# Kernel tuning notes

Measured on AMD Instinct MI355X. Metric: run time of the kernel, lower is better.

The kernel has to match this reference:

```python
import jax, jax.numpy as jnp
import numpy as np

KS = 7       # neighborhood kernel size (fixed in __init__)
HEADS = 8    # num_heads (fixed in __init__)
LN_EPS = 1e-5


def _nbr_idx(L, k):
    # NATTEN-style clamped window: window start shifts inward at borders (no padding)
    starts = jnp.clip(jnp.arange(L) - k // 2, 0, L - k)
    idx = starts[:, None] + jnp.arange(k)            # [L, k] absolute neighbor coords
    rel = idx - jnp.arange(L)[:, None] + (k - 1)     # [L, k] rel-pos-bias index in [0, 2k-2]
    return idx, rel


def _na2d(x, qkv_w, qkv_b, proj_w, proj_b, rpb):
    # x: [B, H, W, C]  -> neighborhood attention with clamped 7x7 windows
    B, H, W, C = x.shape
    hd = C // HEADS
    qkv = x @ qkv_w.T + qkv_b                        # [B,H,W,3C]
    q, k, v = jnp.split(qkv, 3, axis=-1)
    q = q.reshape(B, H, W, HEADS, hd) * (hd ** -0.5)
    k = k.reshape(B, H, W, HEADS, hd)
    v = v.reshape(B, H, W, HEADS, hd)
    ri, rri = _nbr_idx(H, KS)                        # [H,KS]
    ci, rci = _nbr_idx(W, KS)                        # [W,KS]
    # gather neighborhoods: [B,H,W,KS,KS,heads,hd]
    kn = k[:, ri[:, None, :, None], ci[None, :, None, :]]
    vn = v[:, ri[:, None, :, None], ci[None, :, None, :]]
    scores = jnp.einsum('bijhd,bijpqhd->bhijpq', q, kn)   # [B,heads,H,W,KS,KS]
    bias = rpb[:, rri[:, None, :, None], rci[None, :, None, :]]  # [heads,H,W,KS,KS]
    scores = scores + bias[None]
    attn = jax.nn.softmax(scores.reshape(B, HEADS, H, W, KS * KS), axis=-1)
    vn = vn.reshape(B, H, W, KS * KS, HEADS, hd)
    out = jnp.einsum('bhijp,bijphd->bijhd', attn, vn)      # [B,H,W,heads,hd]
    out = out.reshape(B, H, W, C)
    return out @ proj_w.T + proj_b


def _layernorm(x, g, b):
    mu = jnp.mean(x, axis=-1, keepdims=True)
    var = jnp.mean((x - mu) ** 2, axis=-1, keepdims=True)
    return (x - mu) * jax.lax.rsqrt(var + LN_EPS) * g + b


def setup_inputs() -> dict:
    key = jax.random.key(0)
    ks = jax.random.split(key, 4)
    B, T, H, W, C = 2, 8, 48, 48, 64
    return {
        'q': jax.random.normal(ks[0], (B, T, H, W, C), dtype=jnp.float32),
        'qkv_w': jax.random.normal(ks[1], (3 * C, C), dtype=jnp.float32) * 0.02,
        'qkv_b': jnp.zeros((3 * C,), jnp.float32),
        'proj_w': jax.random.normal(ks[2], (C, C), dtype=jnp.float32) * 0.02,
        'proj_b': jnp.zeros((C,), jnp.float32),
        'rpb': jax.random.normal(ks[3], (HEADS, 2 * KS - 1, 2 * KS - 1), dtype=jnp.float32) * 0.02,
        'ln_g': jnp.ones((C,), jnp.float32),
        'ln_b': jnp.zeros((C,), jnp.float32),
    }


def reference(q, qkv_w, qkv_b, proj_w, proj_b, rpb, ln_g, ln_b):
    B, T, H, W, C = q.shape
    x = q.reshape(B * T, H, W, C)                    # '(b t) h w c'
    x = _na2d(x, qkv_w, qkv_b, proj_w, proj_b, rpb)  # wPT path
    x = x.reshape(B, T, H, W, C)
    return _layernorm(x, ln_g, ln_b)                 # norm_q; wGC=False
```

## Files before the change

### kernel.cpp

```cpp
#include <hip/hip_runtime.h>
#include <hip/hip_bf16.h>

#define BT   16
#define IH   48
#define IW   48
#define CH   64
#define NH   8
#define HD   8
#define KS   7
#define NPIX (BT*IH*IW)
#define QKVC 192
#define LN_EPS 1e-5f
#define QSCALE 0.35355339059327373f

#define TSH  4
#define TSW  8
#define TP   (TSH*TSW)
#define AOS  72

typedef __bf16 bf16_t;
typedef bf16_t bf16x8 __attribute__((ext_vector_type(8)));
typedef float  f32x4  __attribute__((ext_vector_type(4)));
typedef float  f32x2  __attribute__((ext_vector_type(2)));

__device__ __forceinline__ float bflo(unsigned u) { union { unsigned i; float f; } v; v.i = u << 16; return v.f; }
__device__ __forceinline__ float bfhi(unsigned u) { union { unsigned i; float f; } v; v.i = u & 0xffff0000u; return v.f; }
__device__ __forceinline__ f32x2 unp2(unsigned u) { f32x2 r; r.x = bflo(u); r.y = bfhi(u); return r; }

__device__ __forceinline__ float4 ldf4u(const float* p) {
    float4 r; __builtin_memcpy(&r, p, 16); return r;
}

__device__ __forceinline__ bf16x8 pack_bf16x8(float4 lo, float4 hi) {
    bf16x8 r;
    r[0] = (bf16_t)lo.x; r[1] = (bf16_t)lo.y; r[2] = (bf16_t)lo.z; r[3] = (bf16_t)lo.w;
    r[4] = (bf16_t)hi.x; r[5] = (bf16_t)hi.y; r[6] = (bf16_t)hi.z; r[7] = (bf16_t)hi.w;
    return r;
}

__global__ __launch_bounds__(192) void qkv_kernel(
        const float* __restrict__ x,
        const float* __restrict__ w,
        const float* __restrict__ b,
        __hip_bfloat16* __restrict__ qkv) {
    const int mg   = blockIdx.x;
    const int ngrp = threadIdx.x >> 6;
    const int l  = threadIdx.x & 63;
    const int m  = l & 15;
    const int kg = l >> 4;

    const int ch_base = ngrp * 64 + m * 4;
    const float4 bias4 = *(const float4*)(b + ch_base);
    const float scale = (ngrp == 0) ? QSCALE : 1.f;

    bf16x8 wb0[4], wb1[4];
    #pragma unroll
    for (int t = 0; t < 4; ++t) {
        const float* wr_ = w + (size_t)(ch_base + t) * CH + kg * 8;
        wb0[t] = pack_bf16x8(*(const float4*)(wr_),      *(const float4*)(wr_ + 4));
        wb1[t] = pack_bf16x8(*(const float4*)(wr_ + 32), *(const float4*)(wr_ + 36));
    }

    #pragma unroll
    for (int mm = 0; mm < 2; ++mm) {
        const int mtile = mg * 2 + mm;
        const float* xr = x + (size_t)(mtile * 16 + m) * CH + kg * 8;
        const bf16x8 a0 = pack_bf16x8(*(const float4*)(xr),      *(const float4*)(xr + 4));
        const bf16x8 a1 = pack_bf16x8(*(const float4*)(xr + 32), *(const float4*)(xr + 36));

        float val[4][4];
        #pragma unroll
        for (int t = 0; t < 4; ++t) {
            f32x4 acc = {0.f, 0.f, 0.f, 0.f};
            acc = __builtin_amdgcn_mfma_f32_16x16x32_bf16(a0, wb0[t], acc, 0, 0, 0);
            acc = __builtin_amdgcn_mfma_f32_16x16x32_bf16(a1, wb1[t], acc, 0, 0, 0);
            const float bias = (t == 0) ? bias4.x : (t == 1) ? bias4.y : (t == 2) ? bias4.z : bias4.w;
            #pragma unroll
            for (int r = 0; r < 4; ++r) val[t][r] = (acc[r] + bias) * scale;
        }
        #pragma unroll
        for (int r = 0; r < 4; ++r) {
            const int pix = mtile * 16 + kg * 4 + r;
            union { ushort4 u; __hip_bfloat16 hh[4]; } pk;
            #pragma unroll
            for (int t = 0; t < 4; ++t) pk.hh[t] = __float2bfloat16(val[t][r]);
            *reinterpret_cast<ushort4*>(qkv + (size_t)pix * QKVC + ch_base) = pk.u;
        }
    }
}

__global__ __launch_bounds__(128) void attn_proj_ln_kernel(
        const __hip_bfloat16* __restrict__ qkv,
        const float* __restrict__ rpb,
        const float* __restrict__ pw,
        const float* __restrict__ pb,
        const float* __restrict__ g,
        const float* __restrict__ beta,
        float* __restrict__ out) {
    __shared__ __align__(16) __hip_bfloat16 ao[TP * AOS];

    const int blk  = blockIdx.x;
    const int n    = blk & 15;
    const int tile = blk >> 4;
    const int i0   = (tile / 6) * TSH;
    const int j0   = (tile % 6) * TSW;
    const int tid  = threadIdx.x;
    const size_t img = (size_t)n * (IH * IW);

    {
        const int h  = tid & 7;
        const int pr = tid >> 3;
        const int pi = pr >> 3;
        const int pj = pr & 7;
        const int i  = i0 + pi * 2;
        const int j  = j0 + pj;
        const int pl0 = pi * 16 + pj;
        const int pl1 = pl0 + 8;

        f32x2 q0[4], q1[4];
        {
            const uint4 u = *reinterpret_cast<const uint4*>(
                qkv + (img + i * IW + j) * QKVC + h * HD);
            q0[0] = unp2(u.x); q0[1] = unp2(u.y); q0[2] = unp2(u.z); q0[3] = unp2(u.w);
            const uint4 v = *reinterpret_cast<const uint4*>(
                qkv + (img + (i + 1) * IW + j) * QKVC + h * HD);
            q1[0] = unp2(v.x); q1[1] = unp2(v.y); q1[2] = unp2(v.z); q1[3] = unp2(v.w);
        }

        int si0 = i - 3;     si0 = si0 < 0 ? 0 : (si0 > IH - KS ? IH - KS : si0);
        int si1 = i - 2;     si1 = si1 < 0 ? 0 : (si1 > IH - KS ? IH - KS : si1);
        int sj  = j - 3;     sj  = sj  < 0 ? 0 : (sj  > IW - KS ? IW - KS : sj);
        const int off    = si1 - si0;
        const int rbase0 = si0 - i + 6;
        const float* rpc = rpb + h * (2*KS-1) * (2*KS-1) + (sj - j + (KS - 1));

        float lr0 = 0.f, lr1 = 0.f;
        f32x2 a0[4], a1[4];
        #pragma unroll
        for (int d = 0; d < 4; ++d) { a0[d] = (f32x2){0.f,0.f}; a1[d] = (f32x2){0.f,0.f}; }

        for (int p = 0; p < 8; ++p) {
            if (p == 7 && off == 0) break;
            const bool d0 = (p < 7);
            const bool d1 = (p > 0) || (off == 0);
            const __hip_bfloat16* row =
                qkv + (img + (si0 + p) * IW + sj) * QKVC + CH + h * HD;

            uint4 kb[KS], vb[KS];
            #pragma unroll
            for (int qq = 0; qq < KS; ++qq) {
                kb[qq] = *reinterpret_cast<const uint4*>(row + qq * QKVC);
                vb[qq] = *reinterpret_cast<const uint4*>(row + qq * QKVC + CH);
            }
            float4 r0a = {0,0,0,0}, r0b = {0,0,0,0}, r1a = {0,0,0,0}, r1b = {0,0,0,0};
            if (d0) {
                const float* rr = rpc + (rbase0 + p) * (2*KS-1);
                r0a = ldf4u(rr); r0b = ldf4u(rr + 3);
            }
            if (d1) {
                const float* rr = rpc + (rbase0 - 1 + p) * (2*KS-1);
                r1a = ldf4u(rr); r1b = ldf4u(rr + 3);
            }

            float s0[KS], s1[KS];
            #pragma unroll
            for (int qq = 0; qq < KS; ++qq) {
                const f32x2 k0 = unp2(kb[qq].x), k1 = unp2(kb[qq].y);
                const f32x2 k2 = unp2(kb[qq].z), k3 = unp2(kb[qq].w);
                f32x2 t0 = q0[0]*k0 + q0[1]*k1 + q0[2]*k2 + q0[3]*k3;
                f32x2 t1 = q1[0]*k0 + q1[1]*k1 + q1[2]*k2 + q1[3]*k3;
                s0[qq] = t0.x + t0.y;
                s1[qq] = t1.x + t1.y;
            }
            float e0[KS], e1[KS];
            #pragma unroll
            for (int qq = 0; qq < KS; ++qq) { e0[qq] = 0.f; e1[qq] = 0.f; }
            if (d0) {
                e0[0] = __expf(s0[0] + r0a.x); e0[1] = __expf(s0[1] + r0a.y);
                e0[2] = __expf(s0[2] + r0a.z); e0[3] = __expf(s0[3] + r0a.w);
                e0[4] = __expf(s0[4] + r0b.y); e0[5] = __expf(s0[5] + r0b.z);
                e0[6] = __expf(s0[6] + r0b.w);
            }
            if (d1) {
                e1[0] = __expf(s1[0] + r1a.x); e1[1] = __expf(s1[1] + r1a.y);
                e1[2] = __expf(s1[2] + r1a.z); e1[3] = __expf(s1[3] + r1a.w);
                e1[4] = __expf(s1[4] + r1b.y); e1[5] = __expf(s1[5] + r1b.z);
                e1[6] = __expf(s1[6] + r1b.w);
            }
            #pragma unroll
            for (int qq = 0; qq < KS; ++qq) {
                const f32x2 v0 = unp2(vb[qq].x), v1 = unp2(vb[qq].y);
                const f32x2 v2 = unp2(vb[qq].z), v3 = unp2(vb[qq].w);
                lr0 += e0[qq];
                a0[0] += e0[qq] * v0; a0[1] += e0[qq] * v1;
                a0[2] += e0[qq] * v2; a0[3] += e0[qq] * v3;
                lr1 += e1[qq];
                a1[0] += e1[qq] * v0; a1[1] += e1[qq] * v1;
                a1[2] += e1[qq] * v2; a1[3] += e1[qq] * v3;
            }
        }
        const float inv0 = 1.f / lr0;
        const float inv1 = 1.f / lr1;
        union { uint4 u; __hip_bfloat16 hh[8]; } pk;
        #pragma unroll
        for (int d = 0; d < 4; ++d) {
            pk.hh[2*d]   = __float2bfloat16(a0[d].x * inv0);
            pk.hh[2*d+1] = __float2bfloat16(a0[d].y * inv0);
        }
        *reinterpret_cast<uint4*>(ao + pl0 * AOS + h * HD) = pk.u;
        #pragma unroll
        for (int d = 0; d < 4; ++d) {
            pk.hh[2*d]   = __float2bfloat16(a1[d].x * inv1);
            pk.hh[2*d+1] = __float2bfloat16(a1[d].y * inv1);
        }
        *reinterpret_cast<uint4*>(ao + pl1 * AOS + h * HD) = pk.u;
    }
    __syncthreads();

    {
        const int wv = tid >> 6;
        const int l  = tid & 63;
        const int m  = l & 15;
        const int kg = l >> 4;

        const __hip_bfloat16* ar = ao + (wv * 16 + m) * AOS + kg * 8;
        const bf16x8 a0 = *reinterpret_cast<const bf16x8*>(ar);
        const bf16x8 a1 = *reinterpret_cast<const bf16x8*>(ar + 32);

        const int ch_base = m * 4;
        const float4 bias4 = *(const float4*)(pb + ch_base);

        float val[4][4];
        #pragma unroll
        for (int t = 0; t < 4; ++t) {
            const float* wr_ = pw + (size_t)(ch_base + t) * CH + kg * 8;
            const bf16x8 b0 = pack_bf16x8(*(const float4*)(wr_),      *(const float4*)(wr_ + 4));
            const bf16x8 b1 = pack_bf16x8(*(const float4*)(wr_ + 32), *(const float4*)(wr_ + 36));
            f32x4 acc = {0.f, 0.f, 0.f, 0.f};
            acc = __builtin_amdgcn_mfma_f32_16x16x32_bf16(a0, b0, acc, 0, 0, 0);
            acc = __builtin_amdgcn_mfma_f32_16x16x32_bf16(a1, b1, acc, 0, 0, 0);
            const float bias = (t == 0) ? bias4.x : (t == 1) ? bias4.y : (t == 2) ? bias4.z : bias4.w;
            #pragma unroll
            for (int r = 0; r < 4; ++r) val[t][r] = acc[r] + bias;
        }

        float sm[4];
        #pragma unroll
        for (int r = 0; r < 4; ++r) sm[r] = val[0][r] + val[1][r] + val[2][r] + val[3][r];
        #pragma unroll
        for (int mask = 1; mask <= 8; mask <<= 1) {
            #pragma unroll
            for (int r = 0; r < 4; ++r) sm[r] += __shfl_xor(sm[r], mask, 64);
        }
        float mu[4];
        #pragma unroll
        for (int r = 0; r < 4; ++r) mu[r] = sm[r] * (1.f / 64.f);

        float qs[4];
        #pragma unroll
        for (int r = 0; r < 4; ++r) {
            float a = val[0][r] - mu[r], bq = val[1][r] - mu[r];
            float c = val[2][r] - mu[r], d = val[3][r] - mu[r];
            qs[r] = a * a + bq * bq + c * c + d * d;
        }
        #pragma unroll
        for (int mask = 1; mask <= 8; mask <<= 1) {
            #pragma unroll
            for (int r = 0; r < 4; ++r) qs[r] += __shfl_xor(qs[r], mask, 64);
        }
        float rs[4];
        #pragma unroll
        for (int r = 0; r < 4; ++r) rs[r] = rsqrtf(qs[r] * (1.f / 64.f) + LN_EPS);

        const float4 g4  = *(const float4*)(g + ch_base);
        const float4 be4 = *(const float4*)(beta + ch_base);
        #pragma unroll
        for (int r = 0; r < 4; ++r) {
            const int pl = wv * 16 + kg * 4 + r;
            const int gi = i0 + (pl >> 3), gj = j0 + (pl & 7);
            float4 o;
            o.x = (val[0][r] - mu[r]) * rs[r] * g4.x + be4.x;
            o.y = (val[1][r] - mu[r]) * rs[r] * g4.y + be4.y;
            o.z = (val[2][r] - mu[r]) * rs[r] * g4.z + be4.z;
            o.w = (val[3][r] - mu[r]) * rs[r] * g4.w + be4.w;
            *reinterpret_cast<float4*>(out + (img + gi * IW + gj) * CH + ch_base) = o;
        }
    }
}

extern "C" void kernel_launch(void* const* d_in, const int* in_sizes, int n_in,
                              void* d_out, int out_size, void* d_ws, size_t ws_size,
                              hipStream_t stream) {
    const float* x      = (const float*)d_in[0];
    const float* qkv_w  = (const float*)d_in[1];
    const float* qkv_b  = (const float*)d_in[2];
    const float* proj_w = (const float*)d_in[3];
    const float* proj_b = (const float*)d_in[4];
    const float* rpb    = (const float*)d_in[5];
    const float* ln_g   = (const float*)d_in[6];
    const float* ln_b   = (const float*)d_in[7];
    float* out = (float*)d_out;

    __hip_bfloat16* qkv = (__hip_bfloat16*)d_ws;

    qkv_kernel<<<1152, 192, 0, stream>>>(x, qkv_w, qkv_b, qkv);
    attn_proj_ln_kernel<<<1152, 128, 0, stream>>>(qkv, rpb, proj_w, proj_b,
                                                  ln_g, ln_b, out);
}
```

Baseline: 111.9 us.

## Fuse QKV projection into attention kernel with halo-recomputed K/V in LDS

Merges the QKV projection and the attention/proj/LayerNorm kernels into one launch that works on 8x8 output tiles. Each block computes Q for its tile and K/V for a 14x14 halo region directly into shared memory, so the bf16 QKV round trip through global memory goes away. In exchange, K/V for halo pixels is recomputed by neighbouring tiles (about 3x redundant projection work), and the larger LDS footprint per block may limit occupancy. Tile size, block size and grid size change to match the new layout.

```diff
diff --git a/kernel.cpp b/kernel.cpp
--- a/kernel.cpp
+++ b/kernel.cpp
@@ -1,21 +1,17 @@
 #include <hip/hip_runtime.h>
 #include <hip/hip_bf16.h>
 
-#define BT   16
 #define IH   48
 #define IW   48
 #define CH   64
-#define NH   8
-#define HD   8
 #define KS   7
-#define NPIX (BT*IH*IW)
-#define QKVC 192
 #define LN_EPS 1e-5f
 #define QSCALE 0.35355339059327373f
 
-#define TSH  4
-#define TSW  8
-#define TP   (TSH*TSW)
+#define TS   8
+#define HS   14
+#define HP   196
+#define KVS  128
 #define AOS  72
 
 typedef __bf16 bf16_t;
@@ -38,74 +34,112 @@
     return r;
 }
 
-__global__ __launch_bounds__(192) void qkv_kernel(
+__global__ __launch_bounds__(256, 2) void fused_na_kernel(
         const float* __restrict__ x,
         const float* __restrict__ w,
         const float* __restrict__ b,
-        __hip_bfloat16* __restrict__ qkv) {
-    const int mg   = blockIdx.x;
-    const int ngrp = threadIdx.x >> 6;
-    const int l  = threadIdx.x & 63;
-    const int m  = l & 15;
-    const int kg = l >> 4;
-
-    const int ch_base = ngrp * 64 + m * 4;
-    const float4 bias4 = *(const float4*)(b + ch_base);
-    const float scale = (ngrp == 0) ? QSCALE : 1.f;
-
-    bf16x8 wb0[4], wb1[4];
-    #pragma unroll
-    for (int t = 0; t < 4; ++t) {
-        const float* wr_ = w + (size_t)(ch_base + t) * CH + kg * 8;
-        wb0[t] = pack_bf16x8(*(const float4*)(wr_),      *(const float4*)(wr_ + 4));
-        wb1[t] = pack_bf16x8(*(const float4*)(wr_ + 32), *(const float4*)(wr_ + 36));
-    }
-
-    #pragma unroll
-    for (int mm = 0; mm < 2; ++mm) {
-        const int mtile = mg * 2 + mm;
-        const float* xr = x + (size_t)(mtile * 16 + m) * CH + kg * 8;
-        const bf16x8 a0 = pack_bf16x8(*(const float4*)(xr),      *(const float4*)(xr + 4));
-        const bf16x8 a1 = pack_bf16x8(*(const float4*)(xr + 32), *(const float4*)(xr + 36));
-
-        float val[4][4];
-        #pragma unroll
-        for (int t = 0; t < 4; ++t) {
-            f32x4 acc = {0.f, 0.f, 0.f, 0.f};
-            acc = __builtin_amdgcn_mfma_f32_16x16x32_bf16(a0, wb0[t], acc, 0, 0, 0);
-            acc = __builtin_amdgcn_mfma_f32_16x16x32_bf16(a1, wb1[t], acc, 0, 0, 0);
-            const float bias = (t == 0) ? bias4.x : (t == 1) ? bias4.y : (t == 2) ? bias4.z : bias4.w;
-            #pragma unroll
-            for (int r = 0; r < 4; ++r) val[t][r] = (acc[r] + bias) * scale;
-        }
-        #pragma unroll
-        for (int r = 0; r < 4; ++r) {
-            const int pix = mtile * 16 + kg * 4 + r;
-            union { ushort4 u; __hip_bfloat16 hh[4]; } pk;
-            #pragma unroll
-            for (int t = 0; t < 4; ++t) pk.hh[t] = __float2bfloat16(val[t][r]);
-            *reinterpret_cast<ushort4*>(qkv + (size_t)pix * QKVC + ch_base) = pk.u;
-        }
-    }
-}
-
-__global__ __launch_bounds__(128) void attn_proj_ln_kernel(
-        const __hip_bfloat16* __restrict__ qkv,
         const float* __restrict__ rpb,
         const float* __restrict__ pw,
         const float* __restrict__ pb,
         const float* __restrict__ g,
         const float* __restrict__ beta,
         float* __restrict__ out) {
-    __shared__ __align__(16) __hip_bfloat16 ao[TP * AOS];
+    __shared__ __align__(16) __hip_bfloat16 kv[HP * KVS];
+    __shared__ __align__(16) __hip_bfloat16 qao[64 * AOS];
 
     const int blk  = blockIdx.x;
     const int n    = blk & 15;
     const int tile = blk >> 4;
-    const int i0   = (tile / 6) * TSH;
-    const int j0   = (tile % 6) * TSW;
-    const int tid  = threadIdx.x;
+    const int i0   = (tile / 6) * TS;
+    const int j0   = (tile % 6) * TS;
+    int h0 = i0 - 3; h0 = h0 < 0 ? 0 : (h0 > IH - HS ? IH - HS : h0);
+    int w0 = j0 - 3; w0 = w0 < 0 ? 0 : (w0 > IW - HS ? IW - HS : w0);
+    const int tid = threadIdx.x;
     const size_t img = (size_t)n * (IH * IW);
+
+    {
+        const int wv = tid >> 6;
+        const int l  = tid & 63;
+        const int m  = l & 15;
+        const int kg = l >> 4;
+
+        {
+            const int ch_base = m * 4;
+            const float4 bias4 = *(const float4*)(b + ch_base);
+            bf16x8 wb0[4], wb1[4];
+            #pragma unroll
+            for (int t = 0; t < 4; ++t) {
+                const float* wr_ = w + (size_t)(ch_base + t) * CH + kg * 8;
+                wb0[t] = pack_bf16x8(*(const float4*)(wr_),      *(const float4*)(wr_ + 4));
+                wb1[t] = pack_bf16x8(*(const float4*)(wr_ + 32), *(const float4*)(wr_ + 36));
+            }
+            const int px = wv * 16 + m;
+            const int hr = i0 + (px >> 3);
+            const int wc = j0 + (px & 7);
+            const float* xr = x + (img + hr * IW + wc) * CH + kg * 8;
+            const bf16x8 a0 = pack_bf16x8(*(const float4*)(xr),      *(const float4*)(xr + 4));
+            const bf16x8 a1 = pack_bf16x8(*(const float4*)(xr + 32), *(const float4*)(xr + 36));
+            float val[4][4];
+            #pragma unroll
+            for (int t = 0; t < 4; ++t) {
+                f32x4 acc = {0.f, 0.f, 0.f, 0.f};
+                acc = __builtin_amdgcn_mfma_f32_16x16x32_bf16(a0, wb0[t], acc, 0, 0, 0);
+                acc = __builtin_amdgcn_mfma_f32_16x16x32_bf16(a1, wb1[t], acc, 0, 0, 0);
+                const float bias = (t == 0) ? bias4.x : (t == 1) ? bias4.y : (t == 2) ? bias4.z : bias4.w;
+                #pragma unroll
+                for (int rr = 0; rr < 4; ++rr) val[t][rr] = (acc[rr] + bias) * QSCALE;
+            }
+            #pragma unroll
+            for (int rr = 0; rr < 4; ++rr) {
+                const int pix = wv * 16 + kg * 4 + rr;
+                union { ushort4 u; __hip_bfloat16 hh[4]; } pk;
+                #pragma unroll
+                for (int t = 0; t < 4; ++t) pk.hh[t] = __float2bfloat16(val[t][rr]);
+                *reinterpret_cast<ushort4*>(qao + pix * 64 + ch_base) = pk.u;
+            }
+        }
+
+        for (int grp = 1; grp < 3; ++grp) {
+            const int ch_base = grp * 64 + m * 4;
+            const float4 bias4 = *(const float4*)(b + ch_base);
+            bf16x8 wb0[4], wb1[4];
+            #pragma unroll
+            for (int t = 0; t < 4; ++t) {
+                const float* wr_ = w + (size_t)(ch_base + t) * CH + kg * 8;
+                wb0[t] = pack_bf16x8(*(const float4*)(wr_),      *(const float4*)(wr_ + 4));
+                wb1[t] = pack_bf16x8(*(const float4*)(wr_ + 32), *(const float4*)(wr_ + 36));
+            }
+            for (int mt = wv; mt < 13; mt += 4) {
+                int hp = mt * 16 + m; if (hp > HP - 1) hp = HP - 1;
+                const int hr = h0 + hp / HS;
+                const int wc = w0 + hp % HS;
+                const float* xr = x + (img + hr * IW + wc) * CH + kg * 8;
+                const bf16x8 a0 = pack_bf16x8(*(const float4*)(xr),      *(const float4*)(xr + 4));
+                const bf16x8 a1 = pack_bf16x8(*(const float4*)(xr + 32), *(const float4*)(xr + 36));
+                float val[4][4];
+                #pragma unroll
+                for (int t = 0; t < 4; ++t) {
+                    f32x4 acc = {0.f, 0.f, 0.f, 0.f};
+                    acc = __builtin_amdgcn_mfma_f32_16x16x32_bf16(a0, wb0[t], acc, 0, 0, 0);
+                    acc = __builtin_amdgcn_mfma_f32_16x16x32_bf16(a1, wb1[t], acc, 0, 0, 0);
+                    const float bias = (t == 0) ? bias4.x : (t == 1) ? bias4.y : (t == 2) ? bias4.z : bias4.w;
+                    #pragma unroll
+                    for (int rr = 0; rr < 4; ++rr) val[t][rr] = acc[rr] + bias;
+                }
+                #pragma unroll
+                for (int rr = 0; rr < 4; ++rr) {
+                    const int pix = mt * 16 + kg * 4 + rr;
+                    if (pix < HP) {
+                        union { ushort4 u; __hip_bfloat16 hh[4]; } pk;
+                        #pragma unroll
+                        for (int t = 0; t < 4; ++t) pk.hh[t] = __float2bfloat16(val[t][rr]);
+                        *reinterpret_cast<ushort4*>(kv + pix * KVS + (grp - 1) * 64 + m * 4) = pk.u;
+                    }
+                }
+            }
+        }
+    }
+    __syncthreads();
 
     {
         const int h  = tid & 7;
@@ -119,13 +153,12 @@
 
         f32x2 q0[4], q1[4];
         {
-            const uint4 u = *reinterpret_cast<const uint4*>(
-                qkv + (img + i * IW + j) * QKVC + h * HD);
+            const uint4 u = *reinterpret_cast<const uint4*>(qao + pl0 * 64 + h * 8);
             q0[0] = unp2(u.x); q0[1] = unp2(u.y); q0[2] = unp2(u.z); q0[3] = unp2(u.w);
-            const uint4 v = *reinterpret_cast<const uint4*>(
-                qkv + (img + (i + 1) * IW + j) * QKVC + h * HD);
+            const uint4 v = *reinterpret_cast<const uint4*>(qao + pl1 * 64 + h * 8);
             q1[0] = unp2(v.x); q1[1] = unp2(v.y); q1[2] = unp2(v.z); q1[3] = unp2(v.w);
         }
+        __syncthreads();
 
         int si0 = i - 3;     si0 = si0 < 0 ? 0 : (si0 > IH - KS ? IH - KS : si0);
         int si1 = i - 2;     si1 = si1 < 0 ? 0 : (si1 > IH - KS ? IH - KS : si1);
@@ -133,6 +166,7 @@
         const int off    = si1 - si0;
         const int rbase0 = si0 - i + 6;
         const float* rpc = rpb + h * (2*KS-1) * (2*KS-1) + (sj - j + (KS - 1));
+        const int c0 = sj - w0;
 
         float lr0 = 0.f, lr1 = 0.f;
         f32x2 a0[4], a1[4];
@@ -143,14 +177,13 @@
             if (p == 7 && off == 0) break;
             const bool d0 = (p < 7);
             const bool d1 = (p > 0) || (off == 0);
-            const __hip_bfloat16* row =
-                qkv + (img + (si0 + p) * IW + sj) * QKVC + CH + h * HD;
+            const __hip_bfloat16* row = kv + ((si0 + p - h0) * HS + c0) * KVS + h * 8;
 
             uint4 kb[KS], vb[KS];
             #pragma unroll
             for (int qq = 0; qq < KS; ++qq) {
-                kb[qq] = *reinterpret_cast<const uint4*>(row + qq * QKVC);
-                vb[qq] = *reinterpret_cast<const uint4*>(row + qq * QKVC + CH);
+                kb[qq] = *reinterpret_cast<const uint4*>(row + qq * KVS);
+                vb[qq] = *reinterpret_cast<const uint4*>(row + qq * KVS + 64);
             }
             float4 r0a = {0,0,0,0}, r0b = {0,0,0,0}, r1a = {0,0,0,0}, r1b = {0,0,0,0};
             if (d0) {
@@ -207,13 +240,13 @@
             pk.hh[2*d]   = __float2bfloat16(a0[d].x * inv0);
             pk.hh[2*d+1] = __float2bfloat16(a0[d].y * inv0);
         }
-        *reinterpret_cast<uint4*>(ao + pl0 * AOS + h * HD) = pk.u;
+        *reinterpret_cast<uint4*>(qao + pl0 * AOS + h * 8) = pk.u;
         #pragma unroll
         for (int d = 0; d < 4; ++d) {
             pk.hh[2*d]   = __float2bfloat16(a1[d].x * inv1);
             pk.hh[2*d+1] = __float2bfloat16(a1[d].y * inv1);
         }
-        *reinterpret_cast<uint4*>(ao + pl1 * AOS + h * HD) = pk.u;
+        *reinterpret_cast<uint4*>(qao + pl1 * AOS + h * 8) = pk.u;
     }
     __syncthreads();
 
@@ -223,7 +256,7 @@
         const int m  = l & 15;
         const int kg = l >> 4;
 
-        const __hip_bfloat16* ar = ao + (wv * 16 + m) * AOS + kg * 8;
+        const __hip_bfloat16* ar = qao + (wv * 16 + m) * AOS + kg * 8;
         const bf16x8 a0 = *reinterpret_cast<const bf16x8*>(ar);
         const bf16x8 a1 = *reinterpret_cast<const bf16x8*>(ar + 32);
 
@@ -301,9 +334,6 @@
     const float* ln_b   = (const float*)d_in[7];
     float* out = (float*)d_out;
 
-    __hip_bfloat16* qkv = (__hip_bfloat16*)d_ws;
-
-    qkv_kernel<<<1152, 192, 0, stream>>>(x, qkv_w, qkv_b, qkv);
-    attn_proj_ln_kernel<<<1152, 128, 0, stream>>>(qkv, rpb, proj_w, proj_b,
-                                                  ln_g, ln_b, out);
+    fused_na_kernel<<<576, 256, 0, stream>>>(x, qkv_w, qkv_b, rpb,
+                                             proj_w, proj_b, ln_g, ln_b, out);
 }
```

Result: slower. 122.9 us (+9.7%).
